# Kernel tuning notes

Hardware: AMD Instinct MI355X
Metric: run time of the kernel (lower is better)

The kernel has to match this reference:

```python
import jax, jax.numpy as jnp
import numpy as np
import math

B, S, D, H = 2, 2048, 1024, 16
DQ = D // H  # d_qkv = 64


def setup_inputs() -> dict:
    key = jax.random.key(0)
    k1, k2, k3, k4 = jax.random.split(key, 4)
    return {
        "Q": jax.random.normal(k1, (B, S, D), dtype=jnp.float32),
        "K": jax.random.normal(k2, (B, S, D), dtype=jnp.float32),
        "V": jax.random.normal(k3, (B, S, D), dtype=jnp.float32),
        "Wo_w": jax.random.normal(k4, (D, D), dtype=jnp.float32) * 0.02,
        "Wo_b": jnp.zeros((D,), dtype=jnp.float32),
        "mask": 1,
    }


def reference(Q, K, V, Wo_w, Wo_b, mask):
    # Note: original module defines Wq/Wk/Wv but never applies them in forward.
    q = Q.reshape(B, S, H, DQ)
    k = K.reshape(B, S, H, DQ)
    v = V.reshape(B, S, H, DQ)
    # raw QK^T scores: [B, H, S, S]
    scores = jnp.einsum("bqhd,bkhd->bhqk", q, k)
    if mask:
        # torch.triu_indices(S, S) default offset=0 -> mask where key >= query
        # (diagonal included). Fill applied BEFORE the sqrt(d) scaling, as in source.
        tri = jnp.arange(S)[:, None] <= jnp.arange(S)[None, :]  # [S, S]
        scores = jnp.where(tri, jnp.float32(-1e9), scores)
    scale = scores / math.sqrt(DQ)
    attn = jax.nn.softmax(scale, axis=-1)
    ctx = jnp.einsum("bhqk,bkhd->bqhd", attn, v).reshape(B, S, D)
    return ctx @ Wo_w.T + Wo_b
```

## Files before the change

kernel.cpp:

```cpp
#include <hip/hip_runtime.h>
#include <hip/hip_bf16.h>
#include <stdint.h>

#define B_  2
#define S_  2048
#define D_  1024
#define H_  16
#define DQ_ 64
#define QT_ (S_/64)
#define FMAX_ 16.0f

typedef float f32x4 __attribute__((ext_vector_type(4)));
typedef short bf16x8 __attribute__((ext_vector_type(8)));

__device__ __forceinline__ unsigned short f2bf(float f) {
    uint32_t u = __float_as_uint(f);
    u += 0x7fffu + ((u >> 16) & 1u);
    return (unsigned short)(u >> 16);
}
__device__ __forceinline__ float bf2f(unsigned short u) {
    return __uint_as_float(((uint32_t)u) << 16);
}

__global__ __launch_bounds__(256) void convert_kernel(
    const float* __restrict__ Q, const float* __restrict__ K,
    const float* __restrict__ W,
    unsigned short* __restrict__ Qb, unsigned short* __restrict__ Kb,
    unsigned short* __restrict__ Wb)
{
    const int n1 = B_*S_*D_/4;
    const int nw = D_*D_/4;
    int i = blockIdx.x*blockDim.x + threadIdx.x;
    if (i >= 2*n1 + nw) return;
    const float* src; unsigned short* dst; int off;
    if (i < n1)        { src = Q; dst = Qb; off = i; }
    else if (i < 2*n1) { src = K; dst = Kb; off = i - n1; }
    else               { src = W; dst = Wb; off = i - 2*n1; }
    float4 f = ((const float4*)src)[off];
    ushort4 o;
    o.x = f2bf(f.x); o.y = f2bf(f.y); o.z = f2bf(f.z); o.w = f2bf(f.w);
    ((ushort4*)dst)[off] = o;
}

__global__ __launch_bounds__(256) void transpose_v_kernel(
    const float* __restrict__ V, unsigned short* __restrict__ Vt,
    float* __restrict__ Pv)
{
    __shared__ unsigned short Ls[64][72];
    const int st = blockIdx.x, h = blockIdx.y, b = blockIdx.z;
    const int tid = threadIdx.x;
    {
        int row = tid >> 2, col0 = (tid & 3) * 16;
        const float* src = V + (((size_t)b*S_ + (size_t)st*64 + row)*D_ + h*64 + col0);
        float4 f0 = ((const float4*)src)[0];
        float4 f1 = ((const float4*)src)[1];
        float4 f2 = ((const float4*)src)[2];
        float4 f3 = ((const float4*)src)[3];
        unsigned short* d = &Ls[row][col0];
        d[0]=f2bf(f0.x); d[1]=f2bf(f0.y); d[2]=f2bf(f0.z); d[3]=f2bf(f0.w);
        d[4]=f2bf(f1.x); d[5]=f2bf(f1.y); d[6]=f2bf(f1.z); d[7]=f2bf(f1.w);
        d[8]=f2bf(f2.x); d[9]=f2bf(f2.y); d[10]=f2bf(f2.z); d[11]=f2bf(f2.w);
        d[12]=f2bf(f3.x); d[13]=f2bf(f3.y); d[14]=f2bf(f3.z); d[15]=f2bf(f3.w);
    }
    __syncthreads();
    {
        int d = tid >> 2, scol = (tid & 3) * 16;
        unsigned short tmp[16];
        float psum = 0.f;
        #pragma unroll
        for (int i = 0; i < 16; ++i) {
            unsigned short u = Ls[scol + i][d];
            tmp[i] = u;
            psum += bf2f(u);
        }
        unsigned short* dst = Vt + ((size_t)((b*H_ + h)*64 + d)*S_ + st*64 + scol);
        ((uint4*)dst)[0] = *((uint4*)tmp);
        ((uint4*)dst)[1] = *((uint4*)(tmp + 8));
        psum += __shfl_xor(psum, 1);
        psum += __shfl_xor(psum, 2);
        if ((tid & 3) == 0)
            Pv[((size_t)(b*H_ + h)*64 + d)*32 + st] = psum;
    }
}

__global__ __launch_bounds__(256) void vmean_kernel(
    const float* __restrict__ Pv, unsigned short* __restrict__ ctx,
    const int* __restrict__ maskp)
{
    if (!maskp[0]) return;
    int idx = blockIdx.x*256 + threadIdx.x;
    int b = idx >> 10, d = idx & 1023;
    const float* p = Pv + ((size_t)(b*H_ + (d >> 6))*64 + (d & 63))*32;
    float s = 0.f;
    #pragma unroll
    for (int i = 0; i < 32; ++i) s += p[i];
    ctx[(size_t)b*S_*D_ + d] = f2bf(s * (1.0f/S_));
}

__global__ __launch_bounds__(256, 2) void attn_kernel(
    const unsigned short* __restrict__ Qb,
    const unsigned short* __restrict__ Kb,
    const unsigned short* __restrict__ Vtb,
    unsigned short* __restrict__ ctx,
    const int* __restrict__ maskp)
{
    __shared__ unsigned short Ks [2][64][72];
    __shared__ unsigned short Vts[2][64][72];
    __shared__ unsigned short Ps [4][16][72];

    const int pa = blockIdx.x, h = blockIdx.y, b = blockIdx.z;
    const int tid  = threadIdx.x;
    const int wave = tid >> 6, lane = tid & 63;
    const int quad = lane >> 4, ln = lane & 15;
    const int maskv = maskp[0];

    const int srow = tid >> 2, scol = (tid & 3)*16;
    const unsigned short* kbase =
        Kb + (((size_t)b*S_ + srow)*D_ + h*64 + scol);
    const unsigned short* vbase =
        Vtb + ((size_t)((b*H_ + h)*64 + srow)*S_ + scol);

    for (int t = 0; t < 2; ++t) {
        const int qt = t ? (QT_-1 - pa) : pa;
        const int niter = maskv ? (qt + 1) : QT_;

        const unsigned short* qrow =
            Qb + (((size_t)b*S_ + (size_t)qt*64 + wave*16 + ln)*D_ + h*64);
        bf16x8 aq0 = *(const bf16x8*)(qrow + quad*8);
        bf16x8 aq1 = *(const bf16x8*)(qrow + 32 + quad*8);

        uint4 k0 = *((const uint4*)(kbase));
        uint4 k1 = *((const uint4*)(kbase + 8));
        uint4 v0 = *((const uint4*)(vbase));
        uint4 v1 = *((const uint4*)(vbase + 8));

        f32x4 o[4] = {};
        float l4[4] = {0.f, 0.f, 0.f, 0.f};
        const int qg = qt*64 + wave*16 + quad*4;

        if (t) __syncthreads();

        for (int j = 0; j < niter; ++j) {
            const int cur = j & 1;
            *((uint4*)&Ks [cur][srow][scol])   = k0;
            *((uint4*)&Ks [cur][srow][scol+8]) = k1;
            *((uint4*)&Vts[cur][srow][scol])   = v0;
            *((uint4*)&Vts[cur][srow][scol+8]) = v1;
            uint4 nk0, nk1, nv0, nv1;
            if (j + 1 < niter) {
                const unsigned short* kp = kbase + (size_t)(j+1)*64*D_;
                const unsigned short* vp = vbase + (j+1)*64;
                nk0 = *((const uint4*)(kp));
                nk1 = *((const uint4*)(kp + 8));
                nv0 = *((const uint4*)(vp));
                nv1 = *((const uint4*)(vp + 8));
            }
            __syncthreads();

            f32x4 s[4] = {};
            #pragma unroll
            for (int nt = 0; nt < 4; ++nt) {
                bf16x8 b0 = *(const bf16x8*)&Ks[cur][nt*16 + ln][quad*8];
                bf16x8 b1 = *(const bf16x8*)&Ks[cur][nt*16 + ln][32 + quad*8];
                s[nt] = __builtin_amdgcn_mfma_f32_16x16x32_bf16(aq0, b0, s[nt], 0,0,0);
                s[nt] = __builtin_amdgcn_mfma_f32_16x16x32_bf16(aq1, b1, s[nt], 0,0,0);
            }

            if (maskv && j == qt) {
                const int kg = j*64 + ln;
                #pragma unroll
                for (int nt = 0; nt < 4; ++nt)
                    #pragma unroll
                    for (int r = 0; r < 4; ++r) {
                        float e = ((kg + nt*16) >= (qg + r)) ? 0.0f
                                   : __expf(s[nt][r]*0.125f - FMAX_);
                        l4[r] += e;
                        Ps[wave][quad*4 + r][nt*16 + ln] = f2bf(e);
                    }
            } else {
                #pragma unroll
                for (int nt = 0; nt < 4; ++nt)
                    #pragma unroll
                    for (int r = 0; r < 4; ++r) {
                        float e = __expf(s[nt][r]*0.125f - FMAX_);
                        l4[r] += e;
                        Ps[wave][quad*4 + r][nt*16 + ln] = f2bf(e);
                    }
            }

            {
                bf16x8 a0 = *(const bf16x8*)&Ps[wave][ln][quad*8];
                bf16x8 a1 = *(const bf16x8*)&Ps[wave][ln][32 + quad*8];
                #pragma unroll
                for (int nt = 0; nt < 4; ++nt) {
                    bf16x8 b0 = *(const bf16x8*)&Vts[cur][nt*16 + ln][quad*8];
                    bf16x8 b1 = *(const bf16x8*)&Vts[cur][nt*16 + ln][32 + quad*8];
                    o[nt] = __builtin_amdgcn_mfma_f32_16x16x32_bf16(a0, b0, o[nt], 0,0,0);
                    o[nt] = __builtin_amdgcn_mfma_f32_16x16x32_bf16(a1, b1, o[nt], 0,0,0);
                }
            }
            k0 = nk0; k1 = nk1; v0 = nv0; v1 = nv1;
        }

        float inv[4];
        #pragma unroll
        for (int r = 0; r < 4; ++r) {
            float lr = l4[r];
            lr += __shfl_xor(lr, 1);
            lr += __shfl_xor(lr, 2);
            lr += __shfl_xor(lr, 4);
            lr += __shfl_xor(lr, 8);
            inv[r] = 1.0f / lr;
        }
        #pragma unroll
        for (int nt = 0; nt < 4; ++nt)
            #pragma unroll
            for (int r = 0; r < 4; ++r) {
                int q = qg + r;
                if (maskv && q == 0) continue;
                int c = h*64 + nt*16 + ln;
                ctx[((size_t)b*S_ + q)*D_ + c] = f2bf(o[nt][r]*inv[r]);
            }
        __syncthreads();
    }
}

__global__ __launch_bounds__(256) void proj_kernel(
    const unsigned short* __restrict__ A,
    const unsigned short* __restrict__ Bw,
    const float* __restrict__ bias,
    float* __restrict__ out)
{
    __shared__ unsigned short As[2][128][72];
    __shared__ unsigned short Bs[2][128][72];
    const int nt0 = blockIdx.x;
    const int mt0 = blockIdx.y;
    const int tid  = threadIdx.x;
    const int wave = tid >> 6, lane = tid & 63;
    const int quad = lane >> 4, ln = lane & 15;
    const int wm = wave >> 1, wn = wave & 1;

    const int srow = tid >> 1, scol = (tid & 1)*32;
    const unsigned short* aptr = A  + ((size_t)(mt0*128 + srow)*1024 + scol);
    const unsigned short* bptr = Bw + ((size_t)(nt0*128 + srow)*1024 + scol);

    uint4 a0 = ((const uint4*)aptr)[0], a1 = ((const uint4*)aptr)[1],
          a2 = ((const uint4*)aptr)[2], a3 = ((const uint4*)aptr)[3];
    uint4 b0 = ((const uint4*)bptr)[0], b1 = ((const uint4*)bptr)[1],
          b2 = ((const uint4*)bptr)[2], b3 = ((const uint4*)bptr)[3];

    f32x4 acc[4][4] = {};

    for (int kt = 0; kt < 16; ++kt) {
        const int cur = kt & 1;
        *((uint4*)&As[cur][srow][scol])    = a0;
        *((uint4*)&As[cur][srow][scol+8])  = a1;
        *((uint4*)&As[cur][srow][scol+16]) = a2;
        *((uint4*)&As[cur][srow][scol+24]) = a3;
        *((uint4*)&Bs[cur][srow][scol])    = b0;
        *((uint4*)&Bs[cur][srow][scol+8])  = b1;
        *((uint4*)&Bs[cur][srow][scol+16]) = b2;
        *((uint4*)&Bs[cur][srow][scol+24]) = b3;
        uint4 na0, na1, na2, na3, nb0, nb1, nb2, nb3;
        if (kt < 15) {
            const unsigned short* ap = aptr + (kt+1)*64;
            const unsigned short* bp = bptr + (kt+1)*64;
            na0 = ((const uint4*)ap)[0]; na1 = ((const uint4*)ap)[1];
            na2 = ((const uint4*)ap)[2]; na3 = ((const uint4*)ap)[3];
            nb0 = ((const uint4*)bp)[0]; nb1 = ((const uint4*)bp)[1];
            nb2 = ((const uint4*)bp)[2]; nb3 = ((const uint4*)bp)[3];
        }
        __syncthreads();
        #pragma unroll
        for (int ks = 0; ks < 2; ++ks) {
            bf16x8 am[4], bn[4];
            #pragma unroll
            for (int i = 0; i < 4; ++i) {
                am[i] = *(const bf16x8*)&As[cur][wm*64 + i*16 + ln][ks*32 + quad*8];
                bn[i] = *(const bf16x8*)&Bs[cur][wn*64 + i*16 + ln][ks*32 + quad*8];
            }
            #pragma unroll
            for (int mi = 0; mi < 4; ++mi)
                #pragma unroll
                for (int ni = 0; ni < 4; ++ni)
                    acc[mi][ni] = __builtin_amdgcn_mfma_f32_16x16x32_bf16(
                        am[mi], bn[ni], acc[mi][ni], 0,0,0);
        }
        a0 = na0; a1 = na1; a2 = na2; a3 = na3;
        b0 = nb0; b1 = nb1; b2 = nb2; b3 = nb3;
    }

    #pragma unroll
    for (int mi = 0; mi < 4; ++mi)
        #pragma unroll
        for (int ni = 0; ni < 4; ++ni) {
            int row = mt0*128 + wm*64 + mi*16 + quad*4;
            int col = nt0*128 + wn*64 + ni*16 + ln;
            float bv = bias[col];
            #pragma unroll
            for (int r = 0; r < 4; ++r)
                out[(size_t)(row + r)*1024 + col] = acc[mi][ni][r] + bv;
        }
}

extern "C" void kernel_launch(void* const* d_in, const int* in_sizes, int n_in,
                              void* d_out, int out_size, void* d_ws, size_t ws_size,
                              hipStream_t stream)
{
    const float* Q   = (const float*)d_in[0];
    const float* K   = (const float*)d_in[1];
    const float* V   = (const float*)d_in[2];
    const float* Wo  = (const float*)d_in[3];
    const float* Wb  = (const float*)d_in[4];
    const int* maskp = (const int*)d_in[5];
    float* out = (float*)d_out;

    unsigned short* Qb   = (unsigned short*)d_ws;
    unsigned short* Kb   = Qb  + (size_t)B_*S_*D_;
    unsigned short* Vtb  = Kb  + (size_t)B_*S_*D_;
    unsigned short* Wob  = Vtb + (size_t)B_*S_*D_;
    unsigned short* ctxb = Wob + (size_t)D_*D_;
    float* Pv = (float*)(ctxb + (size_t)B_*S_*D_);

    int total4 = (2*B_*S_*D_ + D_*D_)/4;
    convert_kernel<<<(total4 + 255)/256, 256, 0, stream>>>(Q, K, Wo, Qb, Kb, Wob);
    transpose_v_kernel<<<dim3(S_/64, H_, B_), 256, 0, stream>>>(V, Vtb, Pv);
    vmean_kernel<<<8, 256, 0, stream>>>(Pv, ctxb, maskp);
    attn_kernel<<<dim3(16, H_, B_), 256, 0, stream>>>(Qb, Kb, Vtb, ctxb, maskp);
    proj_kernel<<<dim3(8, 32), 256, 0, stream>>>(ctxb, Wob, Wb, out);
}
```

Baseline: 168.9 us.

## Fuse prep kernels, convert Q inside attention, and retile output projection

Merges the K/W conversion and V transpose into one prep kernel and folds the V-mean row into the attention kernel, cutting the launch count from five to three. Q is now read as fp32 and converted to bf16 inside attention, so the Q bf16 round trip through memory is gone. The attention grid is flattened with head/batch in the low bits, which changes block scheduling order. The projection GEMM tile drops from 128x128 to 64x128 with two blocks per CU, doubling the grid to give more parallelism.

```diff
diff --git a/kernel.cpp b/kernel.cpp
--- a/kernel.cpp
+++ b/kernel.cpp
@@ -21,86 +21,78 @@
 __device__ __forceinline__ float bf2f(unsigned short u) {
     return __uint_as_float(((uint32_t)u) << 16);
 }
-
-__global__ __launch_bounds__(256) void convert_kernel(
-    const float* __restrict__ Q, const float* __restrict__ K,
+__device__ __forceinline__ bf16x8 packbf8(float4 a, float4 b) {
+    bf16x8 r;
+    r[0]=(short)f2bf(a.x); r[1]=(short)f2bf(a.y);
+    r[2]=(short)f2bf(a.z); r[3]=(short)f2bf(a.w);
+    r[4]=(short)f2bf(b.x); r[5]=(short)f2bf(b.y);
+    r[6]=(short)f2bf(b.z); r[7]=(short)f2bf(b.w);
+    return r;
+}
+
+__global__ __launch_bounds__(256) void prep_kernel(
+    const float* __restrict__ K, const float* __restrict__ V,
     const float* __restrict__ W,
-    unsigned short* __restrict__ Qb, unsigned short* __restrict__ Kb,
-    unsigned short* __restrict__ Wb)
-{
-    const int n1 = B_*S_*D_/4;
-    const int nw = D_*D_/4;
-    int i = blockIdx.x*blockDim.x + threadIdx.x;
-    if (i >= 2*n1 + nw) return;
-    const float* src; unsigned short* dst; int off;
-    if (i < n1)        { src = Q; dst = Qb; off = i; }
-    else if (i < 2*n1) { src = K; dst = Kb; off = i - n1; }
-    else               { src = W; dst = Wb; off = i - 2*n1; }
-    float4 f = ((const float4*)src)[off];
-    ushort4 o;
-    o.x = f2bf(f.x); o.y = f2bf(f.y); o.z = f2bf(f.z); o.w = f2bf(f.w);
-    ((ushort4*)dst)[off] = o;
-}
-
-__global__ __launch_bounds__(256) void transpose_v_kernel(
-    const float* __restrict__ V, unsigned short* __restrict__ Vt,
-    float* __restrict__ Pv)
+    unsigned short* __restrict__ Kb, unsigned short* __restrict__ Vt,
+    unsigned short* __restrict__ Wb, float* __restrict__ Pv)
 {
     __shared__ unsigned short Ls[64][72];
-    const int st = blockIdx.x, h = blockIdx.y, b = blockIdx.z;
-    const int tid = threadIdx.x;
-    {
-        int row = tid >> 2, col0 = (tid & 3) * 16;
-        const float* src = V + (((size_t)b*S_ + (size_t)st*64 + row)*D_ + h*64 + col0);
-        float4 f0 = ((const float4*)src)[0];
-        float4 f1 = ((const float4*)src)[1];
-        float4 f2 = ((const float4*)src)[2];
-        float4 f3 = ((const float4*)src)[3];
-        unsigned short* d = &Ls[row][col0];
-        d[0]=f2bf(f0.x); d[1]=f2bf(f0.y); d[2]=f2bf(f0.z); d[3]=f2bf(f0.w);
-        d[4]=f2bf(f1.x); d[5]=f2bf(f1.y); d[6]=f2bf(f1.z); d[7]=f2bf(f1.w);
-        d[8]=f2bf(f2.x); d[9]=f2bf(f2.y); d[10]=f2bf(f2.z); d[11]=f2bf(f2.w);
-        d[12]=f2bf(f3.x); d[13]=f2bf(f3.y); d[14]=f2bf(f3.z); d[15]=f2bf(f3.w);
+    const int blk = blockIdx.x, tid = threadIdx.x;
+
+    if (blk < 1024) {
+        const int st = blk & 31, h = (blk >> 5) & 15, b = blk >> 9;
+        {
+            int row = tid >> 2, col0 = (tid & 3) * 16;
+            const float* src = V + (((size_t)b*S_ + (size_t)st*64 + row)*D_ + h*64 + col0);
+            float4 f0 = ((const float4*)src)[0];
+            float4 f1 = ((const float4*)src)[1];
+            float4 f2 = ((const float4*)src)[2];
+            float4 f3 = ((const float4*)src)[3];
+            unsigned short* d = &Ls[row][col0];
+            d[0]=f2bf(f0.x); d[1]=f2bf(f0.y); d[2]=f2bf(f0.z); d[3]=f2bf(f0.w);
+            d[4]=f2bf(f1.x); d[5]=f2bf(f1.y); d[6]=f2bf(f1.z); d[7]=f2bf(f1.w);
+            d[8]=f2bf(f2.x); d[9]=f2bf(f2.y); d[10]=f2bf(f2.z); d[11]=f2bf(f2.w);
+            d[12]=f2bf(f3.x); d[13]=f2bf(f3.y); d[14]=f2bf(f3.z); d[15]=f2bf(f3.w);
+        }
+        __syncthreads();
+        {
+            int d = tid >> 2, scol = (tid & 3) * 16;
+            unsigned short tmp[16];
+            float psum = 0.f;
+            #pragma unroll
+            for (int i = 0; i < 16; ++i) {
+                unsigned short u = Ls[scol + i][d];
+                tmp[i] = u;
+                psum += bf2f(u);
+            }
+            unsigned short* dst = Vt + ((size_t)((b*H_ + h)*64 + d)*S_ + st*64 + scol);
+            ((uint4*)dst)[0] = *((uint4*)tmp);
+            ((uint4*)dst)[1] = *((uint4*)(tmp + 8));
+            psum += __shfl_xor(psum, 1);
+            psum += __shfl_xor(psum, 2);
+            if ((tid & 3) == 0)
+                Pv[((size_t)(b*H_ + h)*64 + d)*32 + st] = psum;
+        }
+    } else if (blk < 5120) {
+        int i = (blk - 1024)*256 + tid;
+        float4 f = ((const float4*)K)[i];
+        ushort4 o;
+        o.x = f2bf(f.x); o.y = f2bf(f.y); o.z = f2bf(f.z); o.w = f2bf(f.w);
+        ((ushort4*)Kb)[i] = o;
+    } else {
+        int i = (blk - 5120)*256 + tid;
+        float4 f = ((const float4*)W)[i];
+        ushort4 o;
+        o.x = f2bf(f.x); o.y = f2bf(f.y); o.z = f2bf(f.z); o.w = f2bf(f.w);
+        ((ushort4*)Wb)[i] = o;
     }
-    __syncthreads();
-    {
-        int d = tid >> 2, scol = (tid & 3) * 16;
-        unsigned short tmp[16];
-        float psum = 0.f;
-        #pragma unroll
-        for (int i = 0; i < 16; ++i) {
-            unsigned short u = Ls[scol + i][d];
-            tmp[i] = u;
-            psum += bf2f(u);
-        }
-        unsigned short* dst = Vt + ((size_t)((b*H_ + h)*64 + d)*S_ + st*64 + scol);
-        ((uint4*)dst)[0] = *((uint4*)tmp);
-        ((uint4*)dst)[1] = *((uint4*)(tmp + 8));
-        psum += __shfl_xor(psum, 1);
-        psum += __shfl_xor(psum, 2);
-        if ((tid & 3) == 0)
-            Pv[((size_t)(b*H_ + h)*64 + d)*32 + st] = psum;
-    }
-}
-
-__global__ __launch_bounds__(256) void vmean_kernel(
-    const float* __restrict__ Pv, unsigned short* __restrict__ ctx,
-    const int* __restrict__ maskp)
-{
-    if (!maskp[0]) return;
-    int idx = blockIdx.x*256 + threadIdx.x;
-    int b = idx >> 10, d = idx & 1023;
-    const float* p = Pv + ((size_t)(b*H_ + (d >> 6))*64 + (d & 63))*32;
-    float s = 0.f;
-    #pragma unroll
-    for (int i = 0; i < 32; ++i) s += p[i];
-    ctx[(size_t)b*S_*D_ + d] = f2bf(s * (1.0f/S_));
 }
 
 __global__ __launch_bounds__(256, 2) void attn_kernel(
-    const unsigned short* __restrict__ Qb,
+    const float* __restrict__ Q,
     const unsigned short* __restrict__ Kb,
     const unsigned short* __restrict__ Vtb,
+    const float* __restrict__ Pv,
     unsigned short* __restrict__ ctx,
     const int* __restrict__ maskp)
 {
@@ -108,11 +100,21 @@
     __shared__ unsigned short Vts[2][64][72];
     __shared__ unsigned short Ps [4][16][72];
 
-    const int pa = blockIdx.x, h = blockIdx.y, b = blockIdx.z;
+    const int bid = blockIdx.x;
+    const int g = bid & 31, pa = bid >> 5;
+    const int h = g & 15, b = g >> 4;
     const int tid  = threadIdx.x;
     const int wave = tid >> 6, lane = tid & 63;
     const int quad = lane >> 4, ln = lane & 15;
     const int maskv = maskp[0];
+
+    if (maskv && pa == 0 && tid < 64) {
+        const float* p = Pv + ((size_t)(b*H_ + h)*64 + tid)*32;
+        float s = 0.f;
+        #pragma unroll
+        for (int i = 0; i < 32; ++i) s += p[i];
+        ctx[(size_t)b*S_*D_ + h*64 + tid] = f2bf(s * (1.0f/S_));
+    }
 
     const int srow = tid >> 2, scol = (tid & 3)*16;
     const unsigned short* kbase =
@@ -124,10 +126,14 @@
         const int qt = t ? (QT_-1 - pa) : pa;
         const int niter = maskv ? (qt + 1) : QT_;
 
-        const unsigned short* qrow =
-            Qb + (((size_t)b*S_ + (size_t)qt*64 + wave*16 + ln)*D_ + h*64);
-        bf16x8 aq0 = *(const bf16x8*)(qrow + quad*8);
-        bf16x8 aq1 = *(const bf16x8*)(qrow + 32 + quad*8);
+        const float* qrow =
+            Q + (((size_t)b*S_ + (size_t)qt*64 + wave*16 + ln)*D_ + h*64);
+        float4 q0 = ((const float4*)(qrow + quad*8))[0];
+        float4 q1 = ((const float4*)(qrow + quad*8))[1];
+        float4 q2 = ((const float4*)(qrow + 32 + quad*8))[0];
+        float4 q3 = ((const float4*)(qrow + 32 + quad*8))[1];
+        bf16x8 aq0 = packbf8(q0, q1);
+        bf16x8 aq1 = packbf8(q2, q3);
 
         uint4 k0 = *((const uint4*)(kbase));
         uint4 k1 = *((const uint4*)(kbase + 8));
@@ -225,77 +231,74 @@
     }
 }
 
-__global__ __launch_bounds__(256) void proj_kernel(
+__global__ __launch_bounds__(256, 2) void proj_kernel(
     const unsigned short* __restrict__ A,
     const unsigned short* __restrict__ Bw,
     const float* __restrict__ bias,
     float* __restrict__ out)
 {
-    __shared__ unsigned short As[2][128][72];
+    __shared__ unsigned short As[2][64][72];
     __shared__ unsigned short Bs[2][128][72];
     const int nt0 = blockIdx.x;
     const int mt0 = blockIdx.y;
     const int tid  = threadIdx.x;
     const int wave = tid >> 6, lane = tid & 63;
     const int quad = lane >> 4, ln = lane & 15;
-    const int wm = wave >> 1, wn = wave & 1;
-
-    const int srow = tid >> 1, scol = (tid & 1)*32;
-    const unsigned short* aptr = A  + ((size_t)(mt0*128 + srow)*1024 + scol);
-    const unsigned short* bptr = Bw + ((size_t)(nt0*128 + srow)*1024 + scol);
-
-    uint4 a0 = ((const uint4*)aptr)[0], a1 = ((const uint4*)aptr)[1],
-          a2 = ((const uint4*)aptr)[2], a3 = ((const uint4*)aptr)[3];
+
+    const int arow = tid >> 2, acol = (tid & 3)*16;
+    const int brow = tid >> 1, bcol = (tid & 1)*32;
+    const unsigned short* aptr = A  + ((size_t)(mt0*64  + arow)*1024 + acol);
+    const unsigned short* bptr = Bw + ((size_t)(nt0*128 + brow)*1024 + bcol);
+
+    uint4 a0 = ((const uint4*)aptr)[0], a1 = ((const uint4*)aptr)[1];
     uint4 b0 = ((const uint4*)bptr)[0], b1 = ((const uint4*)bptr)[1],
           b2 = ((const uint4*)bptr)[2], b3 = ((const uint4*)bptr)[3];
 
-    f32x4 acc[4][4] = {};
+    f32x4 acc[4][2] = {};
 
     for (int kt = 0; kt < 16; ++kt) {
         const int cur = kt & 1;
-        *((uint4*)&As[cur][srow][scol])    = a0;
-        *((uint4*)&As[cur][srow][scol+8])  = a1;
-        *((uint4*)&As[cur][srow][scol+16]) = a2;
-        *((uint4*)&As[cur][srow][scol+24]) = a3;
-        *((uint4*)&Bs[cur][srow][scol])    = b0;
-        *((uint4*)&Bs[cur][srow][scol+8])  = b1;
-        *((uint4*)&Bs[cur][srow][scol+16]) = b2;
-        *((uint4*)&Bs[cur][srow][scol+24]) = b3;
-        uint4 na0, na1, na2, na3, nb0, nb1, nb2, nb3;
+        *((uint4*)&As[cur][arow][acol])    = a0;
+        *((uint4*)&As[cur][arow][acol+8])  = a1;
+        *((uint4*)&Bs[cur][brow][bcol])    = b0;
+        *((uint4*)&Bs[cur][brow][bcol+8])  = b1;
+        *((uint4*)&Bs[cur][brow][bcol+16]) = b2;
+        *((uint4*)&Bs[cur][brow][bcol+24]) = b3;
+        uint4 na0, na1, nb0, nb1, nb2, nb3;
         if (kt < 15) {
             const unsigned short* ap = aptr + (kt+1)*64;
             const unsigned short* bp = bptr + (kt+1)*64;
             na0 = ((const uint4*)ap)[0]; na1 = ((const uint4*)ap)[1];
-            na2 = ((const uint4*)ap)[2]; na3 = ((const uint4*)ap)[3];
             nb0 = ((const uint4*)bp)[0]; nb1 = ((const uint4*)bp)[1];
             nb2 = ((const uint4*)bp)[2]; nb3 = ((const uint4*)bp)[3];
         }
         __syncthreads();
         #pragma unroll
         for (int ks = 0; ks < 2; ++ks) {
-            bf16x8 am[4], bn[4];
-            #pragma unroll
-            for (int i = 0; i < 4; ++i) {
-                am[i] = *(const bf16x8*)&As[cur][wm*64 + i*16 + ln][ks*32 + quad*8];
-                bn[i] = *(const bf16x8*)&Bs[cur][wn*64 + i*16 + ln][ks*32 + quad*8];
-            }
+            bf16x8 am[4], bn[2];
+            #pragma unroll
+            for (int i = 0; i < 4; ++i)
+                am[i] = *(const bf16x8*)&As[cur][i*16 + ln][ks*32 + quad*8];
+            #pragma unroll
+            for (int i = 0; i < 2; ++i)
+                bn[i] = *(const bf16x8*)&Bs[cur][wave*32 + i*16 + ln][ks*32 + quad*8];
             #pragma unroll
             for (int mi = 0; mi < 4; ++mi)
                 #pragma unroll
-                for (int ni = 0; ni < 4; ++ni)
+                for (int ni = 0; ni < 2; ++ni)
                     acc[mi][ni] = __builtin_amdgcn_mfma_f32_16x16x32_bf16(
                         am[mi], bn[ni], acc[mi][ni], 0,0,0);
         }
-        a0 = na0; a1 = na1; a2 = na2; a3 = na3;
+        a0 = na0; a1 = na1;
         b0 = nb0; b1 = nb1; b2 = nb2; b3 = nb3;
     }
 
     #pragma unroll
     for (int mi = 0; mi < 4; ++mi)
         #pragma unroll
-        for (int ni = 0; ni < 4; ++ni) {
-            int row = mt0*128 + wm*64 + mi*16 + quad*4;
-            int col = nt0*128 + wn*64 + ni*16 + ln;
+        for (int ni = 0; ni < 2; ++ni) {
+            int row = mt0*64 + mi*16 + quad*4;
+            int col = nt0*128 + wave*32 + ni*16 + ln;
             float bv = bias[col];
             #pragma unroll
             for (int r = 0; r < 4; ++r)
@@ -315,17 +318,13 @@
     const int* maskp = (const int*)d_in[5];
     float* out = (float*)d_out;
 
-    unsigned short* Qb   = (unsigned short*)d_ws;
-    unsigned short* Kb   = Qb  + (size_t)B_*S_*D_;
+    unsigned short* Kb   = (unsigned short*)d_ws;
     unsigned short* Vtb  = Kb  + (size_t)B_*S_*D_;
     unsigned short* Wob  = Vtb + (size_t)B_*S_*D_;
     unsigned short* ctxb = Wob + (size_t)D_*D_;
     float* Pv = (float*)(ctxb + (size_t)B_*S_*D_);
 
-    int total4 = (2*B_*S_*D_ + D_*D_)/4;
-    convert_kernel<<<(total4 + 255)/256, 256, 0, stream>>>(Q, K, Wo, Qb, Kb, Wob);
-    transpose_v_kernel<<<dim3(S_/64, H_, B_), 256, 0, stream>>>(V, Vtb, Pv);
-    vmean_kernel<<<8, 256, 0, stream>>>(Pv, ctxb, maskp);
-    attn_kernel<<<dim3(16, H_, B_), 256, 0, stream>>>(Qb, Kb, Vtb, ctxb, maskp);
-    proj_kernel<<<dim3(8, 32), 256, 0, stream>>>(ctxb, Wob, Wb, out);
-}
+    prep_kernel<<<6144, 256, 0, stream>>>(K, V, Wo, Kb, Vtb, Wob, Pv);
+    attn_kernel<<<512, 256, 0, stream>>>(Q, Kb, Vtb, Pv, ctxb, maskp);
+    proj_kernel<<<dim3(8, 64), 256, 0, stream>>>(ctxb, Wob, Wb, out);
+}
```

After: 154.2 us. -8.7%, faster.
